# Optimization experiments

Hardware: AMD Instinct MI355X
Metric: run time of the kernel (lower is better)

The kernel has to match this reference:

```python
import jax, jax.numpy as jnp
import numpy as np

B, N, H = 8, 2000, 64  # batch, num_nodes(=input_dim), hidden(num_gru_units)


def _laplacian_self_loop(a):
    # batched: norm = D^{-1/2} (A + I) D^{-1/2}
    m = a + jnp.eye(a.shape[-1], dtype=a.dtype)
    d_inv_sqrt = jnp.sum(m, axis=-1) ** -0.5  # (B, N)
    return d_inv_sqrt[..., :, None] * m * d_inv_sqrt[..., None, :]


def _graph_conv(inputs, hidden_flat, adj, windd, W2, b2, W3, b3, W, b, out_dim):
    b_, _, n = inputs.shape
    # dynamic wind-based adjacency
    wind_now = inputs[:, 2, :] * 360.0  # (B, N)
    direction = jnp.abs(windd[None, :, :] - wind_now[:, :, None])  # (B, N, N)
    direction = jnp.where(direction > 360.0, 180.0, direction)
    d1 = jnp.maximum(jnp.cos(direction * (jnp.pi / 180.0)), 0.0)
    a = d1 @ W2.T + b2 + (adj @ W3.T + b3)[None]  # (B, N, N)
    a1 = _laplacian_self_loop(jnp.maximum(a, 0.0))
    # graph conv: concat [x, h] then A @ [.] then Linear
    x = jnp.concatenate([inputs[:, 0, :, None], hidden_flat.reshape(b_, n, H)], axis=2)  # (B,N,H+1)
    y = jnp.einsum('bij,bjh->bih', a1, x) @ W.T + b  # (B, N, out_dim)
    return y.reshape(b_, n * out_dim)


def reference(inputs, hidden_state, adj, windd, W2, b2, W3, b3, W1a, b1a, W1b, b1b, Wca1, Wca2, Wsa):
    b_, _, n = inputs.shape
    conc = _graph_conv(inputs, hidden_state, adj, windd, W2, b2, W3, b3, W1a, b1a, 2 * H)
    conc = conc.reshape(b_, 2 * H, n)  # faithful reshape (input_dim == N)
    # --- channel attention (CBAM) ---
    avg = jnp.mean(conc, axis=2, keepdims=True)  # (B, 2H, 1)
    mx = jnp.max(conc, axis=2, keepdims=True)
    def fc(v):
        return jnp.einsum('oc,bcx->box', Wca2, jax.nn.relu(jnp.einsum('oc,bcx->box', Wca1, v)))
    ca = jax.nn.sigmoid(fc(avg) + fc(mx))  # (B, 2H, 1)
    conc = ca * conc
    # --- spatial attention ---
    s = jnp.stack([jnp.mean(conc, axis=1), jnp.max(conc, axis=1)], axis=1)  # (B, 2, N)
    sa = jax.lax.conv_general_dilated(s, Wsa, window_strides=(1,), padding=((3, 3),),
                                      dimension_numbers=('NCH', 'OIH', 'NCH'))  # (B,1,N)
    conc = jax.nn.sigmoid(sa) * conc
    # --- GRU gates ---
    conc = jax.nn.sigmoid(conc.reshape(b_, 2 * H * n))
    r, u = jnp.split(conc, 2, axis=1)  # each (B, N*H)
    c = jnp.tanh(_graph_conv(inputs, r * hidden_state, adj, windd, W2, b2, W3, b3, W1b, b1b, H))
    new_hidden_state = u * hidden_state + (1.0 - u) * c
    return new_hidden_state


def setup_inputs() -> dict:
    key = jax.random.key(0)
    ks = jax.random.split(key, 12)
    inputs = jax.random.uniform(ks[0], (B, 3, N), dtype=jnp.float32)
    hidden_state = jax.random.normal(ks[1], (B, N * H), dtype=jnp.float32) * 0.1
    adj = jax.random.uniform(ks[2], (N, N), dtype=jnp.float32)
    windd = jax.random.uniform(ks[3], (N, N), dtype=jnp.float32) * 360.0
    sN = 1.0 / np.sqrt(N)
    W2 = jax.random.normal(ks[4], (N, N), dtype=jnp.float32) * sN
    b2 = jnp.zeros((N,), jnp.float32)
    W3 = jax.random.normal(ks[5], (N, N), dtype=jnp.float32) * sN
    b3 = jnp.zeros((N,), jnp.float32)
    sI = 1.0 / np.sqrt(H + 1)
    W1a = jax.random.normal(ks[6], (2 * H, H + 1), dtype=jnp.float32) * sI
    b1a = jnp.ones((2 * H,), jnp.float32)  # bias=1.0 in graph_conv1
    W1b = jax.random.normal(ks[7], (H, H + 1), dtype=jnp.float32) * sI
    b1b = jnp.zeros((H,), jnp.float32)
    Wca1 = jax.random.normal(ks[8], (2 * H // 16, 2 * H), dtype=jnp.float32) * (1.0 / np.sqrt(2 * H))
    Wca2 = jax.random.normal(ks[9], (2 * H, 2 * H // 16), dtype=jnp.float32) * (1.0 / np.sqrt(2 * H // 16))
    Wsa = jax.random.normal(ks[10], (1, 2, 7), dtype=jnp.float32) * (1.0 / np.sqrt(14))
    return {'inputs': inputs, 'hidden_state': hidden_state, 'adj': adj, 'windd': windd,
            'W2': W2, 'b2': b2, 'W3': W3, 'b3': b3, 'W1a': W1a, 'b1a': b1a,
            'W1b': W1b, 'b1b': b1b, 'Wca1': Wca1, 'Wca2': Wca2, 'Wsa': Wsa}
```

## Files before the change

### kernel.cpp

```cpp
#include <hip/hip_runtime.h>

#define NN 2000
#define BB 8
#define P  2048
#define NIT 32

typedef __attribute__((ext_vector_type(8))) short bf16x8;
typedef __attribute__((ext_vector_type(4))) float f32x4;

__device__ __forceinline__ float sigf(float x) { return 1.0f / (1.0f + expf(-x)); }

__device__ __forceinline__ short f2bf(float x) {
    union { float f; unsigned u; } v; v.f = x;
    unsigned r = v.u + 0x7fffu + ((v.u >> 16) & 1u);
    return (short)(r >> 16);
}
__device__ __forceinline__ float bf2f(short h) {
    union { unsigned u; float f; } v; v.u = ((unsigned)(unsigned short)h) << 16; return v.f;
}

__device__ __forceinline__ void gl2lds16(const short* g, short* l) {
    __builtin_amdgcn_global_load_lds(
        (const __attribute__((address_space(1))) void*)g,
        (__attribute__((address_space(3))) void*)l, 16, 0, 0);
}

__global__ __launch_bounds__(256) void k_cvt(
    const float* __restrict__ W2, const float* __restrict__ W3,
    const float* __restrict__ adj, const float* __restrict__ windd,
    const float* __restrict__ inputs,
    short* __restrict__ W2bf, short* __restrict__ W3bf,
    short* __restrict__ adjbf, short* __restrict__ d1bf)
{
    const int i = blockIdx.x, sel = blockIdx.y, t = threadIdx.x;
    const bool live = (i < NN) && (t < 250);
    if (sel < 3) {
        const float* s = (sel == 0) ? W2 : (sel == 1) ? W3 : adj;
        short* d = ((sel == 0) ? W2bf : (sel == 1) ? W3bf : adjbf) + ((size_t)i) * P + t * 8;
        bf16x8 v;
#pragma unroll
        for (int e = 0; e < 8; ++e) v[e] = 0;
        if (live) {
            const float* p = s + (size_t)i * NN + t * 8;
            float4 x0 = *(const float4*)p;
            float4 x1 = *(const float4*)(p + 4);
            float a[8] = {x0.x,x0.y,x0.z,x0.w,x1.x,x1.y,x1.z,x1.w};
#pragma unroll
            for (int e = 0; e < 8; ++e) v[e] = f2bf(a[e]);
        }
        *(bf16x8*)d = v;
    } else {
        float a[8];
        if (live) {
            const float* p = windd + (size_t)i * NN + t * 8;
            float4 x0 = *(const float4*)p;
            float4 x1 = *(const float4*)(p + 4);
            a[0]=x0.x; a[1]=x0.y; a[2]=x0.z; a[3]=x0.w;
            a[4]=x1.x; a[5]=x1.y; a[6]=x1.z; a[7]=x1.w;
        }
#pragma unroll
        for (int b = 0; b < BB; ++b) {
            bf16x8 v;
#pragma unroll
            for (int e = 0; e < 8; ++e) v[e] = 0;
            if (live) {
                const float wn = inputs[(size_t)b * 3 * NN + 2 * NN + i] * 360.0f;
#pragma unroll
                for (int e = 0; e < 8; ++e) {
                    float dd = fabsf(a[e] - wn);
                    dd = (dd > 360.0f) ? 180.0f : dd;
                    float c = __cosf(dd * 0.01745329251994329577f);
                    v[e] = f2bf(fmaxf(c, 0.0f));
                }
            }
            *(bf16x8*)(d1bf + ((size_t)b * P + i) * P + t * 8) = v;
        }
    }
}

__global__ __launch_bounds__(512, 2) void k_gd(
    const short* __restrict__ d1bf, const short* __restrict__ W2bf,
    const float* __restrict__ b2, const short* __restrict__ adjw,
    short* __restrict__ m_bf, float* __restrict__ rowpart)
{
    __shared__ char smem[131072];
    const int t = threadIdx.x;
    const int w = t >> 6, lane = t & 63;
    const int wm = w >> 2, wn = w & 3;
    const int lr = lane & 15, lq = lane >> 4;
    const int tile = blockIdx.x;
    const int b = blockIdx.y;
    const int i0 = (tile & 7) * 256;
    const int j0 = (tile >> 3) * 256;
    const short* A  = d1bf + (size_t)b * P * P;
    const short* Bm = W2bf;

    const short* srcA[4];
    const short* srcB[4];
#pragma unroll
    for (int q = 0; q < 4; ++q) {
        const int c = q * 512 + t;
        const int r = c >> 3;
        const int g = (c & 7) ^ (r & 7);
        srcA[q] = A  + (size_t)(i0 + r) * P + g * 8;
        srcB[q] = Bm + (size_t)(j0 + r) * P + g * 8;
    }

#define STAGE_ALL(slot, ktI) do {                                                      \
        gl2lds16(srcA[0] + (ktI) * 64, (short*)(smem + (slot) * 32768 + (w * 64) * 16));          \
        gl2lds16(srcA[1] + (ktI) * 64, (short*)(smem + (slot) * 32768 + (512 + w * 64) * 16));    \
        gl2lds16(srcA[2] + (ktI) * 64, (short*)(smem + (slot) * 32768 + (1024 + w * 64) * 16));   \
        gl2lds16(srcA[3] + (ktI) * 64, (short*)(smem + (slot) * 32768 + (1536 + w * 64) * 16));   \
        gl2lds16(srcB[0] + (ktI) * 64, (short*)(smem + 65536 + (slot) * 32768 + (w * 64) * 16));          \
        gl2lds16(srcB[1] + (ktI) * 64, (short*)(smem + 65536 + (slot) * 32768 + (512 + w * 64) * 16));    \
        gl2lds16(srcB[2] + (ktI) * 64, (short*)(smem + 65536 + (slot) * 32768 + (1024 + w * 64) * 16));   \
        gl2lds16(srcB[3] + (ktI) * 64, (short*)(smem + 65536 + (slot) * 32768 + (1536 + w * 64) * 16)); } while (0)

    const int fx0 = (lq << 4) ^ ((lr & 7) << 4);
    const int fx1 = ((4 + lq) << 4) ^ ((lr & 7) << 4);
    const int arowB = (wm * 128 + lr) * 128;
    const int browB = (wn * 64 + lr) * 128;

    f32x4 acc[8][4];
#pragma unroll
    for (int m = 0; m < 8; ++m)
#pragma unroll
        for (int n = 0; n < 4; ++n) acc[m][n] = (f32x4){0.f, 0.f, 0.f, 0.f};
    bf16x8 aF[4][2], bF[4][2];

    STAGE_ALL(0, 0);
    asm volatile("s_waitcnt vmcnt(0)" ::: "memory");
    __builtin_amdgcn_s_barrier();
    asm volatile("" ::: "memory");

#define MFMA_(a_, b_, m, n) acc[m][n] = __builtin_amdgcn_mfma_f32_16x16x32_bf16(a_, b_, acc[m][n], 0, 0, 0)

    for (int kt = 0; kt < NIT; ++kt) {
        char* curA = smem + (kt & 1) * 32768;
        char* curB = smem + 65536 + (kt & 1) * 32768;
        const int stgSlot = (kt + 1) & 1;
        const int stgKt = (kt + 1 < NIT) ? (kt + 1) : (NIT - 1);

        STAGE_ALL(stgSlot, stgKt);

#pragma unroll
        for (int m = 0; m < 4; ++m) {
            aF[m][0] = *(const bf16x8*)(curA + arowB + m * 2048 + fx0);
            aF[m][1] = *(const bf16x8*)(curA + arowB + m * 2048 + fx1);
        }
#pragma unroll
        for (int n = 0; n < 4; ++n) {
            bF[n][0] = *(const bf16x8*)(curB + browB + n * 2048 + fx0);
            bF[n][1] = *(const bf16x8*)(curB + browB + n * 2048 + fx1);
        }
        asm volatile("s_waitcnt lgkmcnt(0)" ::: "memory");
        __builtin_amdgcn_sched_barrier(0);
        __builtin_amdgcn_s_setprio(1);
#pragma unroll
        for (int m = 0; m < 4; ++m)
#pragma unroll
            for (int n = 0; n < 4; ++n) {
                MFMA_(aF[m][0], bF[n][0], m, n);
                MFMA_(aF[m][1], bF[n][1], m, n);
            }
        __builtin_amdgcn_s_setprio(0);

#pragma unroll
        for (int m = 0; m < 4; ++m) {
            aF[m][0] = *(const bf16x8*)(curA + arowB + (m + 4) * 2048 + fx0);
            aF[m][1] = *(const bf16x8*)(curA + arowB + (m + 4) * 2048 + fx1);
        }
        asm volatile("s_waitcnt lgkmcnt(0)" ::: "memory");
        __builtin_amdgcn_sched_barrier(0);
        __builtin_amdgcn_s_setprio(1);
#pragma unroll
        for (int m = 0; m < 4; ++m)
#pragma unroll
            for (int n = 0; n < 4; ++n) {
                MFMA_(aF[m][0], bF[n][0], m + 4, n);
                MFMA_(aF[m][1], bF[n][1], m + 4, n);
            }
        __builtin_amdgcn_s_setprio(0);

        asm volatile("s_waitcnt vmcnt(0)" ::: "memory");
        __builtin_amdgcn_s_barrier();
        asm volatile("" ::: "memory");
    }

    const int rbase = i0 + wm * 128 + lq * 4;
    const int cbase = j0 + wn * 64 + lr;
    float* red = (float*)smem;
#pragma unroll
    for (int m = 0; m < 8; ++m) {
#pragma unroll
        for (int q = 0; q < 4; ++q) {
            const int row = rbase + m * 16 + q;
            float rs = 0.0f;
#pragma unroll
            for (int n = 0; n < 4; ++n) {
                const int col = cbase + n * 16;
                short o = 0;
                if (row < NN && col < NN) {
                    float x = acc[m][n][q] + b2[col] + bf2f(adjw[(size_t)row * NN + col]);
                    x = fmaxf(x, 0.0f);
                    if (row == col) x += 1.0f;
                    o = f2bf(x);
                    rs += x;
                }
                m_bf[((size_t)b * P + row) * P + col] = o;
            }
            red[(wm * 128 + m * 16 + lq * 4 + q) * 66 + (wn * 16 + lr)] = rs;
        }
    }
    __syncthreads();
    if (t < 256) {
        const float* rr = red + t * 66;
        float s = 0.0f;
#pragma unroll
        for (int k2 = 0; k2 < 64; ++k2) s += rr[k2];
        const int row = i0 + t;
        if (row < NN)
            rowpart[((size_t)b * 8 + (tile >> 3)) * 2048 + row] = s;
    }
#undef MFMA_
#undef STAGE_ALL
}

__global__ __launch_bounds__(256) void k_dinv(const float* __restrict__ rowpart,
                                              float* __restrict__ dinv)
{
    const int t = blockIdx.x * 256 + threadIdx.x;
    if (t >= BB * NN) return;
    const int b = t / NN, i = t % NN;
    float s = 0.0f;
#pragma unroll
    for (int jt = 0; jt < 8; ++jt)
        s += rowpart[((size_t)b * 8 + jt) * 2048 + i];
    dinv[t] = rsqrtf(s);
}

template<int EPI, int OUTD>
__global__ __launch_bounds__(256) void k_mfma(
    const short* __restrict__ Abase, const short* __restrict__ Bbase,
    const float* __restrict__ bias, const short* __restrict__ adjw,
    void* __restrict__ Cout, short* __restrict__ part, size_t aBatch)
{
    __shared__ short shA[4096];
    __shared__ short shB[4096];
    const int t = threadIdx.x;
    const int w = t >> 6, lane = t & 63;
    const int wr = w >> 1, wc = w & 1;

    int i0, j0, b, kt = 0;
    if (EPI == 2) {
        i0 = blockIdx.x * 128; j0 = 0; kt = blockIdx.y; b = blockIdx.z;
    } else {
        i0 = blockIdx.x * 128; j0 = blockIdx.y * 128; b = 0;
    }
    const int kb = (EPI == 2) ? kt * (P / 4) : 0;
    const int ke = (EPI == 2) ? kt * (P / 4) + (P / 4) : P;

    const short* A  = Abase + (size_t)b * aBatch;
    const short* Bm = Bbase + ((EPI == 2) ? (size_t)b * 128 * P : (size_t)0);

    f32x4 acc[4][4];
#pragma unroll
    for (int m = 0; m < 4; ++m)
#pragma unroll
        for (int n = 0; n < 4; ++n) acc[m][n] = (f32x4){0.f, 0.f, 0.f, 0.f};

    const int lidx0 = w * 128 + lane;
    const int lidx1 = lidx0 + 64;
    const short* aS0 = A  + (size_t)(i0 + (lidx0 >> 2)) * P + (lidx0 & 3) * 8;
    const short* aS1 = A  + (size_t)(i0 + (lidx1 >> 2)) * P + (lidx1 & 3) * 8;
    const short* bS0 = Bm + (size_t)(j0 + (lidx0 >> 2)) * P + (lidx0 & 3) * 8;
    const short* bS1 = Bm + (size_t)(j0 + (lidx1 >> 2)) * P + (lidx1 & 3) * 8;
    short* ldA0 = shA + (w * 128) * 8;
    short* ldA1 = shA + (w * 128 + 64) * 8;
    short* ldB0 = shB + (w * 128) * 8;
    short* ldB1 = shB + (w * 128 + 64) * 8;

    const int lr = lane & 15, lq = lane >> 4;
    const int aoff = (wr * 64 + lr) * 32 + lq * 8;
    const int boff = (wc * 64 + lr) * 32 + lq * 8;

    for (int k0 = kb; k0 < ke; k0 += 32) {
        gl2lds16(aS0 + k0, ldA0);
        gl2lds16(aS1 + k0, ldA1);
        gl2lds16(bS0 + k0, ldB0);
        gl2lds16(bS1 + k0, ldB1);
        __syncthreads();
        bf16x8 aF[4], bF[4];
#pragma unroll
        for (int m = 0; m < 4; ++m) aF[m] = *(const bf16x8*)(shA + aoff + m * 512);
#pragma unroll
        for (int n = 0; n < 4; ++n) bF[n] = *(const bf16x8*)(shB + boff + n * 512);
#pragma unroll
        for (int m = 0; m < 4; ++m)
#pragma unroll
            for (int n = 0; n < 4; ++n)
                acc[m][n] = __builtin_amdgcn_mfma_f32_16x16x32_bf16(aF[m], bF[n], acc[m][n], 0, 0, 0);
        __syncthreads();
    }

    const int rbase = i0 + wr * 64 + lq * 4;
    const int cbase = j0 + wc * 64 + lr;
#pragma unroll
    for (int m = 0; m < 4; ++m) {
#pragma unroll
        for (int n = 0; n < 4; ++n) {
            const int col = cbase + n * 16;
#pragma unroll
            for (int q = 0; q < 4; ++q) {
                const int row = rbase + m * 16 + q;
                float v = acc[m][n][q];
                if (EPI == 0) {
                    if (row < NN && col < NN)
                        ((short*)Cout)[(size_t)row * NN + col] = f2bf(v + bias[col]);
                } else {
                    if (row < NN && col < OUTD)
                        part[((size_t)(kt * BB + b) * NN + row) * OUTD + col] = f2bf(v);
                }
            }
        }
    }
}

template<int OUTD>
__global__ __launch_bounds__(256) void k_comb(
    const short* __restrict__ part, const float* __restrict__ dinv,
    const float* __restrict__ bias, float* __restrict__ out)
{
    const size_t idx = (size_t)blockIdx.x * 256 + threadIdx.x;
    const size_t S = (size_t)BB * NN * OUTD;
    if (idx >= S) return;
    const int o = (int)(idx % OUTD);
    const size_t r = idx / OUTD;
    const int i = (int)(r % NN);
    const int b = (int)(r / NN);
    float s = (bf2f(part[idx]) + bf2f(part[idx + S])) +
              (bf2f(part[idx + 2 * S]) + bf2f(part[idx + 3 * S]));
    out[idx] = s * dinv[b * NN + i] + bias[o];
}

__global__ __launch_bounds__(256) void k_cfin(
    const short* __restrict__ part, const float* __restrict__ dinv,
    const float* __restrict__ bias, const float* __restrict__ u,
    const float* __restrict__ hidden, float* __restrict__ out)
{
    const size_t idx = (size_t)blockIdx.x * 256 + threadIdx.x;
    const size_t S = (size_t)BB * NN * 64;
    if (idx >= S) return;
    const int o = (int)(idx & 63);
    const size_t r = idx >> 6;
    const int i = (int)(r % NN);
    const int b = (int)(r / NN);
    float s = (bf2f(part[idx]) + bf2f(part[idx + S])) +
              (bf2f(part[idx + 2 * S]) + bf2f(part[idx + 3 * S]));
    float c = tanhf(s * dinv[b * NN + i] + bias[o]);
    float uu = u[idx];
    out[idx] = uu * hidden[idx] + (1.0f - uu) * c;
}

template<int OUT>
__global__ __launch_bounds__(128) void k_xwT(
    const float* __restrict__ inputs, const float* __restrict__ hsrc,
    const float* __restrict__ W, const float* __restrict__ dinv, short* __restrict__ zT)
{
    const int b = blockIdx.y;
    const int j0 = blockIdx.x * 16;
    const int t = threadIdx.x;
    __shared__ float wl[128 * 65];
    __shared__ float xs[16 * 66];
    __shared__ float dj[16];
    for (int idx = t; idx < OUT * 65; idx += 128) wl[idx] = W[idx];
    for (int idx = t; idx < 16 * 64; idx += 128) {
        int jj = idx >> 6, hh = idx & 63, j = j0 + jj;
        xs[jj * 66 + 1 + hh] = (j < NN) ? hsrc[((size_t)b * NN + j) * 64 + hh] : 0.0f;
    }
    if (t < 16) {
        int j = j0 + t;
        xs[t * 66] = (j < NN) ? inputs[(size_t)b * 3 * NN + j] : 0.0f;
        dj[t] = (j < NN) ? dinv[b * NN + j] : 0.0f;
    }
    __syncthreads();
    for (int jj = 0; jj < 16; ++jj) {
        float a = 0.0f;
        if (t < OUT) {
            const float* xr = &xs[jj * 66];
            const float* wr = &wl[t * 65];
#pragma unroll
            for (int c = 0; c < 65; ++c) a = fmaf(xr[c], wr[c], a);
        }
        int j = j0 + jj;
        zT[((size_t)b * 128 + t) * P + j] = (t < OUT && j < NN) ? f2bf(a * dj[jj]) : (short)0;
    }
}

__global__ __launch_bounds__(256) void k_chred(const float* __restrict__ conc,
                                               float* __restrict__ avg, float* __restrict__ mx)
{
    const int bc = blockIdx.x;
    const float* p = conc + (size_t)bc * NN;
    float s = 0.0f, mv = -3.402823466e+38f;
    for (int n = threadIdx.x; n < NN; n += 256) { float v = p[n]; s += v; mv = fmaxf(mv, v); }
#pragma unroll
    for (int off = 32; off > 0; off >>= 1) {
        s += __shfl_down(s, off);
        mv = fmaxf(mv, __shfl_down(mv, off));
    }
    __shared__ float rs[4], rm[4];
    if ((threadIdx.x & 63) == 0) { rs[threadIdx.x >> 6] = s; rm[threadIdx.x >> 6] = mv; }
    __syncthreads();
    if (threadIdx.x == 0) {
        avg[bc] = (rs[0] + rs[1] + rs[2] + rs[3]) * (1.0f / NN);
        mx[bc]  = fmaxf(fmaxf(rm[0], rm[1]), fmaxf(rm[2], rm[3]));
    }
}

__global__ __launch_bounds__(128) void k_ca(
    const float* __restrict__ avg, const float* __restrict__ mx,
    const float* __restrict__ Wca1, const float* __restrict__ Wca2, float* __restrict__ ca)
{
    const int b = blockIdx.x, t = threadIdx.x;
    __shared__ float av[128], mv[128], h[16];
    av[t] = avg[b * 128 + t];
    mv[t] = mx[b * 128 + t];
    __syncthreads();
    if (t < 16) {
        int o8 = t & 7;
        const float* src = (t < 8) ? av : mv;
        float s = 0.0f;
        for (int c = 0; c < 128; ++c) s = fmaf(Wca1[o8 * 128 + c], src[c], s);
        h[t] = fmaxf(s, 0.0f);
    }
    __syncthreads();
    float s = 0.0f;
#pragma unroll
    for (int k = 0; k < 8; ++k) s = fmaf(Wca2[t * 8 + k], h[k] + h[8 + k], s);
    ca[b * 128 + t] = sigf(s);
}

__global__ __launch_bounds__(256) void k_satgate(
    const float* __restrict__ conc, const float* __restrict__ ca,
    const float* __restrict__ Wsa, const float* __restrict__ hidden,
    float* __restrict__ rh, float* __restrict__ u)
{
    const int b = blockIdx.y;
    const int n0 = blockIdx.x * 256;
    const int t = threadIdx.x;
    __shared__ float cas[128];
    __shared__ float wsa[14];
    __shared__ float s0l[262], s1l[262];
    if (t < 128) cas[t] = ca[b * 128 + t];
    if (t >= 128 && t < 142) wsa[t - 128] = Wsa[t - 128];
    __syncthreads();

    const float* cb = conc + (size_t)b * NN * 128;
    {
        const int n = n0 + t;
        float sm = 0.0f, sx = -3.402823466e+38f;
        if (n < NN) {
            for (int c = 0; c < 128; ++c) {
                float v = cas[c] * cb[(size_t)c * NN + n];
                sm += v; sx = fmaxf(sx, v);
            }
            s0l[t + 3] = sm * (1.0f / 128.0f);
            s1l[t + 3] = sx;
        } else { s0l[t + 3] = 0.0f; s1l[t + 3] = 0.0f; }
    }
    if (t < 6) {
        const int hn = (t < 3) ? (n0 - 3 + t) : (n0 + 256 + (t - 3));
        const int hi = (t < 3) ? t : (256 + t);
        float sm = 0.0f, sx = -3.402823466e+38f;
        if (hn >= 0 && hn < NN) {
            for (int c = 0; c < 128; ++c) {
                float v = cas[c] * cb[(size_t)c * NN + hn];
                sm += v; sx = fmaxf(sx, v);
            }
            s0l[hi] = sm * (1.0f / 128.0f);
            s1l[hi] = sx;
        } else { s0l[hi] = 0.0f; s1l[hi] = 0.0f; }
    }
    __syncthreads();

    const int n = n0 + t;
    if (n >= NN) return;
    float sa = 0.0f;
#pragma unroll
    for (int k = 0; k < 7; ++k)
        sa += wsa[k] * s0l[t + k] + wsa[7 + k] * s1l[t + k];
    float gs = sigf(sa);
    for (int c = 0; c < 128; ++c) {
        float v = gs * cas[c] * cb[(size_t)c * NN + n];
        float g = sigf(v);
        if (c < 64)
            rh[(size_t)b * NN * 64 + (size_t)c * NN + n] =
                g * hidden[(size_t)b * NN * 64 + (size_t)c * NN + n];
        else
            u[(size_t)b * NN * 64 + (size_t)(c - 64) * NN + n] = g;
    }
}

extern "C" void kernel_launch(void* const* d_in, const int* in_sizes, int n_in,
                              void* d_out, int out_size, void* d_ws, size_t ws_size,
                              hipStream_t stream)
{
    (void)in_sizes; (void)n_in; (void)out_size; (void)ws_size;
    const float* inputs = (const float*)d_in[0];
    const float* hidden = (const float*)d_in[1];
    const float* adj    = (const float*)d_in[2];
    const float* windd  = (const float*)d_in[3];
    const float* W2     = (const float*)d_in[4];
    const float* b2     = (const float*)d_in[5];
    const float* W3     = (const float*)d_in[6];
    const float* b3     = (const float*)d_in[7];
    const float* W1a    = (const float*)d_in[8];
    const float* b1a    = (const float*)d_in[9];
    const float* W1b    = (const float*)d_in[10];
    const float* b1b    = (const float*)d_in[11];
    const float* Wca1   = (const float*)d_in[12];
    const float* Wca2   = (const float*)d_in[13];
    const float* Wsa    = (const float*)d_in[14];
    float* out = (float*)d_out;

    char* W = (char*)d_ws;
    short* adjW3bf = (short*)(W + 0);
    short* W2bf    = (short*)(W + 8000000);
    short* W3bf    = (short*)(W + 16388608);
    short* adjbf   = (short*)(W + 24777216);
    short* m_bf    = (short*)(W + 16388608);
    char* D = W + 83497472;
    short* d1bf = (short*)D;
    float* dinv = (float*)(D + 0);
    float* avgb = (float*)(D + 64000);
    float* mxb  = (float*)(D + 68096);
    float* cab  = (float*)(D + 72192);
    short* zT   = (short*)(D + 204800);
    float* conc = (float*)(D + 4399104);
    float* rh   = (float*)(D + 12591104);
    float* ubuf = (float*)(D + 16687104);
    short* part = (short*)(D + 24879104);
    float* rowpart = (float*)(D + 67108864);

    const size_t PP = (size_t)P * P;

    k_cvt<<<dim3(P, 4), 256, 0, stream>>>(W2, W3, adj, windd, inputs,
                                          W2bf, W3bf, adjbf, d1bf);
    k_mfma<0, 0><<<dim3(16, 16, 1), 256, 0, stream>>>(adjbf, W3bf, b3, nullptr, adjW3bf, nullptr, 0);
    k_gd<<<dim3(64, BB), 512, 0, stream>>>(d1bf, W2bf, b2, adjW3bf, m_bf, rowpart);
    k_dinv<<<(BB * NN + 255) / 256, 256, 0, stream>>>(rowpart, dinv);
    k_xwT<128><<<dim3(128, BB), 128, 0, stream>>>(inputs, hidden, W1a, dinv, zT);
    k_mfma<2, 128><<<dim3(16, 4, BB), 256, 0, stream>>>(m_bf, zT, nullptr, nullptr, nullptr, part, PP);
    k_comb<128><<<(BB * NN * 128 + 255) / 256, 256, 0, stream>>>(part, dinv, b1a, conc);
    k_chred<<<BB * 128, 256, 0, stream>>>(conc, avgb, mxb);
    k_ca<<<BB, 128, 0, stream>>>(avgb, mxb, Wca1, Wca2, cab);
    k_satgate<<<dim3(8, BB), 256, 0, stream>>>(conc, cab, Wsa, hidden, rh, ubuf);
    k_xwT<64><<<dim3(128, BB), 128, 0, stream>>>(inputs, rh, W1b, dinv, zT);
    k_mfma<2, 64><<<dim3(16, 4, BB), 256, 0, stream>>>(m_bf, zT, nullptr, nullptr, nullptr, part, PP);
    k_cfin<<<(BB * NN * 64 + 255) / 256, 256, 0, stream>>>(part, dinv, b1b, ubuf, hidden, out);
}
```

Baseline: 403.0 us.

## Fuse small elementwise and reduction kernels to cut launches and conc re-reads

Three small kernels are folded into neighbours. The degree rsqrt (k_dinv) now runs inside k_xwT<128>. The partial-sum combine is merged with the per-channel mean/max reduction into one block-per-channel kernel. The channel-attention MLP is recomputed at the start of each k_satgate block. This drops three launches and one full read of conc, at the cost of redundant CA MLP work per block and one block per (channel, batch) in the combine kernel.

```diff
diff --git a/kernel.cpp b/kernel.cpp
--- a/kernel.cpp
+++ b/kernel.cpp
@@ -226,19 +226,6 @@
 #undef STAGE_ALL
 }
 
-__global__ __launch_bounds__(256) void k_dinv(const float* __restrict__ rowpart,
-                                              float* __restrict__ dinv)
-{
-    const int t = blockIdx.x * 256 + threadIdx.x;
-    if (t >= BB * NN) return;
-    const int b = t / NN, i = t % NN;
-    float s = 0.0f;
-#pragma unroll
-    for (int jt = 0; jt < 8; ++jt)
-        s += rowpart[((size_t)b * 8 + jt) * 2048 + i];
-    dinv[t] = rsqrtf(s);
-}
-
 template<int EPI, int OUTD>
 __global__ __launch_bounds__(256) void k_mfma(
     const short* __restrict__ Abase, const short* __restrict__ Bbase,
@@ -326,21 +313,37 @@
     }
 }
 
-template<int OUTD>
-__global__ __launch_bounds__(256) void k_comb(
+__global__ __launch_bounds__(256) void k_combred(
     const short* __restrict__ part, const float* __restrict__ dinv,
-    const float* __restrict__ bias, float* __restrict__ out)
-{
-    const size_t idx = (size_t)blockIdx.x * 256 + threadIdx.x;
-    const size_t S = (size_t)BB * NN * OUTD;
-    if (idx >= S) return;
-    const int o = (int)(idx % OUTD);
-    const size_t r = idx / OUTD;
-    const int i = (int)(r % NN);
-    const int b = (int)(r / NN);
-    float s = (bf2f(part[idx]) + bf2f(part[idx + S])) +
-              (bf2f(part[idx + 2 * S]) + bf2f(part[idx + 3 * S]));
-    out[idx] = s * dinv[b * NN + i] + bias[o];
+    const float* __restrict__ bias, float* __restrict__ conc,
+    float* __restrict__ avg, float* __restrict__ mx)
+{
+    const int c = blockIdx.x, b = blockIdx.y, t = threadIdx.x;
+    const size_t S = (size_t)BB * NN * 128;
+    const size_t base = (size_t)b * NN * 128;
+    float sm = 0.0f, sx = -3.402823466e+38f;
+    for (int n = t; n < NN; n += 256) {
+        const size_t f = (size_t)c * NN + n;
+        const int i = (int)(f >> 7), o = (int)(f & 127);
+        const size_t pidx = base + f;
+        float s = (bf2f(part[pidx]) + bf2f(part[pidx + S])) +
+                  (bf2f(part[pidx + 2 * S]) + bf2f(part[pidx + 3 * S]));
+        float v = s * dinv[b * NN + i] + bias[o];
+        conc[pidx] = v;
+        sm += v; sx = fmaxf(sx, v);
+    }
+#pragma unroll
+    for (int off = 32; off > 0; off >>= 1) {
+        sm += __shfl_down(sm, off);
+        sx = fmaxf(sx, __shfl_down(sx, off));
+    }
+    __shared__ float rs[4], rm[4];
+    if ((t & 63) == 0) { rs[t >> 6] = sm; rm[t >> 6] = sx; }
+    __syncthreads();
+    if (t == 0) {
+        avg[b * 128 + c] = (rs[0] + rs[1] + rs[2] + rs[3]) * (1.0f / NN);
+        mx[b * 128 + c]  = fmaxf(fmaxf(rm[0], rm[1]), fmaxf(rm[2], rm[3]));
+    }
 }
 
 __global__ __launch_bounds__(256) void k_cfin(
@@ -365,7 +368,8 @@
 template<int OUT>
 __global__ __launch_bounds__(128) void k_xwT(
     const float* __restrict__ inputs, const float* __restrict__ hsrc,
-    const float* __restrict__ W, const float* __restrict__ dinv, short* __restrict__ zT)
+    const float* __restrict__ W, const float* __restrict__ rowpart,
+    float* __restrict__ dinv, short* __restrict__ zT)
 {
     const int b = blockIdx.y;
     const int j0 = blockIdx.x * 16;
@@ -381,7 +385,20 @@
     if (t < 16) {
         int j = j0 + t;
         xs[t * 66] = (j < NN) ? inputs[(size_t)b * 3 * NN + j] : 0.0f;
-        dj[t] = (j < NN) ? dinv[b * NN + j] : 0.0f;
+        float dv = 0.0f;
+        if (j < NN) {
+            if (OUT == 128) {
+                float s = 0.0f;
+#pragma unroll
+                for (int jt = 0; jt < 8; ++jt)
+                    s += rowpart[((size_t)b * 8 + jt) * 2048 + j];
+                dv = rsqrtf(s);
+                dinv[b * NN + j] = dv;
+            } else {
+                dv = dinv[b * NN + j];
+            }
+        }
+        dj[t] = dv;
     }
     __syncthreads();
     for (int jj = 0; jj < 16; ++jj) {
@@ -397,35 +414,20 @@
     }
 }
 
-__global__ __launch_bounds__(256) void k_chred(const float* __restrict__ conc,
-                                               float* __restrict__ avg, float* __restrict__ mx)
-{
-    const int bc = blockIdx.x;
-    const float* p = conc + (size_t)bc * NN;
-    float s = 0.0f, mv = -3.402823466e+38f;
-    for (int n = threadIdx.x; n < NN; n += 256) { float v = p[n]; s += v; mv = fmaxf(mv, v); }
-#pragma unroll
-    for (int off = 32; off > 0; off >>= 1) {
-        s += __shfl_down(s, off);
-        mv = fmaxf(mv, __shfl_down(mv, off));
-    }
-    __shared__ float rs[4], rm[4];
-    if ((threadIdx.x & 63) == 0) { rs[threadIdx.x >> 6] = s; rm[threadIdx.x >> 6] = mv; }
-    __syncthreads();
-    if (threadIdx.x == 0) {
-        avg[bc] = (rs[0] + rs[1] + rs[2] + rs[3]) * (1.0f / NN);
-        mx[bc]  = fmaxf(fmaxf(rm[0], rm[1]), fmaxf(rm[2], rm[3]));
-    }
-}
-
-__global__ __launch_bounds__(128) void k_ca(
-    const float* __restrict__ avg, const float* __restrict__ mx,
-    const float* __restrict__ Wca1, const float* __restrict__ Wca2, float* __restrict__ ca)
-{
-    const int b = blockIdx.x, t = threadIdx.x;
-    __shared__ float av[128], mv[128], h[16];
-    av[t] = avg[b * 128 + t];
-    mv[t] = mx[b * 128 + t];
+__global__ __launch_bounds__(256) void k_satgate(
+    const float* __restrict__ conc, const float* __restrict__ avg,
+    const float* __restrict__ mxv, const float* __restrict__ Wca1,
+    const float* __restrict__ Wca2, const float* __restrict__ Wsa,
+    const float* __restrict__ hidden, float* __restrict__ rh, float* __restrict__ u)
+{
+    const int b = blockIdx.y;
+    const int n0 = blockIdx.x * 256;
+    const int t = threadIdx.x;
+    __shared__ float av[128], mv[128], h[16], cas[128];
+    __shared__ float wsa[14];
+    __shared__ float s0l[262], s1l[262];
+    if (t < 128) { av[t] = avg[b * 128 + t]; mv[t] = mxv[b * 128 + t]; }
+    if (t >= 128 && t < 142) wsa[t - 128] = Wsa[t - 128];
     __syncthreads();
     if (t < 16) {
         int o8 = t & 7;
@@ -435,25 +437,12 @@
         h[t] = fmaxf(s, 0.0f);
     }
     __syncthreads();
-    float s = 0.0f;
-#pragma unroll
-    for (int k = 0; k < 8; ++k) s = fmaf(Wca2[t * 8 + k], h[k] + h[8 + k], s);
-    ca[b * 128 + t] = sigf(s);
-}
-
-__global__ __launch_bounds__(256) void k_satgate(
-    const float* __restrict__ conc, const float* __restrict__ ca,
-    const float* __restrict__ Wsa, const float* __restrict__ hidden,
-    float* __restrict__ rh, float* __restrict__ u)
-{
-    const int b = blockIdx.y;
-    const int n0 = blockIdx.x * 256;
-    const int t = threadIdx.x;
-    __shared__ float cas[128];
-    __shared__ float wsa[14];
-    __shared__ float s0l[262], s1l[262];
-    if (t < 128) cas[t] = ca[b * 128 + t];
-    if (t >= 128 && t < 142) wsa[t - 128] = Wsa[t - 128];
+    if (t < 128) {
+        float s = 0.0f;
+#pragma unroll
+        for (int k = 0; k < 8; ++k) s = fmaf(Wca2[t * 8 + k], h[k] + h[8 + k], s);
+        cas[t] = sigf(s);
+    }
     __syncthreads();
 
     const float* cb = conc + (size_t)b * NN * 128;
@@ -535,7 +524,6 @@
     float* dinv = (float*)(D + 0);
     float* avgb = (float*)(D + 64000);
     float* mxb  = (float*)(D + 68096);
-    float* cab  = (float*)(D + 72192);
     short* zT   = (short*)(D + 204800);
     float* conc = (float*)(D + 4399104);
     float* rh   = (float*)(D + 12591104);
@@ -549,14 +537,11 @@
                                           W2bf, W3bf, adjbf, d1bf);
     k_mfma<0, 0><<<dim3(16, 16, 1), 256, 0, stream>>>(adjbf, W3bf, b3, nullptr, adjW3bf, nullptr, 0);
     k_gd<<<dim3(64, BB), 512, 0, stream>>>(d1bf, W2bf, b2, adjW3bf, m_bf, rowpart);
-    k_dinv<<<(BB * NN + 255) / 256, 256, 0, stream>>>(rowpart, dinv);
-    k_xwT<128><<<dim3(128, BB), 128, 0, stream>>>(inputs, hidden, W1a, dinv, zT);
+    k_xwT<128><<<dim3(128, BB), 128, 0, stream>>>(inputs, hidden, W1a, rowpart, dinv, zT);
     k_mfma<2, 128><<<dim3(16, 4, BB), 256, 0, stream>>>(m_bf, zT, nullptr, nullptr, nullptr, part, PP);
-    k_comb<128><<<(BB * NN * 128 + 255) / 256, 256, 0, stream>>>(part, dinv, b1a, conc);
-    k_chred<<<BB * 128, 256, 0, stream>>>(conc, avgb, mxb);
-    k_ca<<<BB, 128, 0, stream>>>(avgb, mxb, Wca1, Wca2, cab);
-    k_satgate<<<dim3(8, BB), 256, 0, stream>>>(conc, cab, Wsa, hidden, rh, ubuf);
-    k_xwT<64><<<dim3(128, BB), 128, 0, stream>>>(inputs, rh, W1b, dinv, zT);
+    k_combred<<<dim3(128, BB), 256, 0, stream>>>(part, dinv, b1a, conc, avgb, mxb);
+    k_satgate<<<dim3(8, BB), 256, 0, stream>>>(conc, avgb, mxb, Wca1, Wca2, Wsa, hidden, rh, ubuf);
+    k_xwT<64><<<dim3(128, BB), 128, 0, stream>>>(inputs, rh, W1b, rowpart, dinv, zT);
     k_mfma<2, 64><<<dim3(16, 4, BB), 256, 0, stream>>>(m_bf, zT, nullptr, nullptr, nullptr, part, PP);
     k_cfin<<<(BB * NN * 64 + 255) / 256, 256, 0, stream>>>(part, dinv, b1b, ubuf, hidden, out);
 }
```

Result: faster. 394.8 us (-2.0%).
